# Kernel optimization log

Measured on AMD Instinct MI355X. Metric: run time of the kernel, lower is better.

The kernel has to match this reference:

```python
import jax, jax.numpy as jnp
import numpy as np

DIM = 1280
HEADS = 16
HEAD_DIM = DIM // HEADS  # 80
SEQ = 2048


def setup_inputs() -> dict:
    key = jax.random.key(0)
    ks = jax.random.split(key, 6)
    hidden_states = jax.random.normal(ks[0], (SEQ, DIM), jnp.float32)
    rotary_pos_emb = jax.random.normal(ks[1], (SEQ, HEAD_DIM // 2), jnp.float32)
    # 4 variable-length windows packed into one flat sequence
    cu_seqlens = jnp.array([0, 512, 1024, 1536, 2048], jnp.int32)
    w_scale = DIM ** -0.5
    qkv_w = jax.random.normal(ks[2], (3 * DIM, DIM), jnp.float32) * w_scale
    qkv_b = jax.random.normal(ks[3], (3 * DIM,), jnp.float32) * 0.01
    proj_w = jax.random.normal(ks[4], (DIM, DIM), jnp.float32) * w_scale
    proj_b = jax.random.normal(ks[5], (DIM,), jnp.float32) * 0.01
    return {
        "hidden_states": hidden_states,
        "rotary_pos_emb": rotary_pos_emb,
        "cu_seqlens": cu_seqlens,
        "qkv_w": qkv_w,
        "qkv_b": qkv_b,
        "proj_w": proj_w,
        "proj_b": proj_b,
    }


def _apply_rope_vision(x, freqs):
    # x: [S, H, D], freqs: [S, D//2]; matches Qwen2-VL apply_rotary_pos_emb_vision
    cos = jnp.concatenate([jnp.cos(freqs), jnp.cos(freqs)], axis=-1)[:, None, :]  # [S,1,D]
    sin = jnp.concatenate([jnp.sin(freqs), jnp.sin(freqs)], axis=-1)[:, None, :]
    x1, x2 = jnp.split(x, 2, axis=-1)
    rot = jnp.concatenate([-x2, x1], axis=-1)  # rotate_half
    return x * cos + rot * sin


def reference(hidden_states, rotary_pos_emb, cu_seqlens, qkv_w, qkv_b, proj_w, proj_b):
    S = hidden_states.shape[0]
    qkv = (hidden_states @ qkv_w.T + qkv_b).reshape(S, 3, HEADS, HEAD_DIM)
    q, k, v = qkv[:, 0], qkv[:, 1], qkv[:, 2]  # each [S, H, D]
    q = _apply_rope_vision(q, rotary_pos_emb)
    k = _apply_rope_vision(k, rotary_pos_emb)
    # varlen attention: tokens attend only within their cu_seqlens window
    seg = jnp.searchsorted(cu_seqlens[1:], jnp.arange(S), side="right")
    mask = seg[:, None] == seg[None, :]  # [S, S]
    scale = HEAD_DIM ** -0.5
    scores = jnp.einsum("shd,thd->hst", q, k) * scale  # [H, S, S]
    scores = jnp.where(mask[None, :, :], scores, jnp.finfo(scores.dtype).min)
    probs = jax.nn.softmax(scores, axis=-1)
    attn = jnp.einsum("hst,thd->shd", probs, v).reshape(S, DIM)
    return attn @ proj_w.T + proj_b
```

## Files before the change

### kernel.cpp

```cpp
#include <hip/hip_runtime.h>


typedef __attribute__((ext_vector_type(8))) short bf16x8;
typedef __attribute__((ext_vector_type(4))) float floatx4;
typedef __attribute__((ext_vector_type(4))) short short4v;
typedef __attribute__((ext_vector_type(8))) short short8v;

static __device__ __forceinline__ short f2bf(float f) {
  union { float f; unsigned u; } v; v.f = f;
  unsigned r = v.u + 0x7FFFu + ((v.u >> 16) & 1u);
  return (short)(r >> 16);
}
static __device__ __forceinline__ float bf2f(short h) {
  union { unsigned u; float f; } v;
  v.u = ((unsigned)(unsigned short)h) << 16;
  return v.f;
}

static __device__ __forceinline__ void gload16(const short* g, short* l) {
  __builtin_amdgcn_global_load_lds(
      (const __attribute__((address_space(1))) unsigned*)g,
      (__attribute__((address_space(3))) unsigned*)l, 16, 0, 0);
}

#define CVT_N1 327680
#define CVT_N2 614400
#define CVT_N3 204800
__global__ __launch_bounds__(256) void cvt3_kernel(const float* __restrict__ s1, short* __restrict__ d1,
                                                   const float* __restrict__ s2, short* __restrict__ d2,
                                                   const float* __restrict__ s3, short* __restrict__ d3) {
  int i = blockIdx.x * 256 + threadIdx.x;
  const float* s; short* d; int j;
  if (i < CVT_N1)                { s = s1; d = d1; j = i; }
  else if (i < CVT_N1 + CVT_N2)  { s = s2; d = d2; j = i - CVT_N1; }
  else                           { s = s3; d = d3; j = i - CVT_N1 - CVT_N2; }
  float4 x = ((const float4*)s)[2 * j];
  float4 y = ((const float4*)s)[2 * j + 1];
  short8v o;
  o[0] = f2bf(x.x); o[1] = f2bf(x.y); o[2] = f2bf(x.z); o[3] = f2bf(x.w);
  o[4] = f2bf(y.x); o[5] = f2bf(y.y); o[6] = f2bf(y.z); o[7] = f2bf(y.w);
  ((short8v*)d)[j] = o;
}

template <int MODE, int BM, int BN>
__global__ __launch_bounds__(256) void gemm_db(const short* __restrict__ A,
                                               const short* __restrict__ B,
                                               const float* __restrict__ bias,
                                               void* __restrict__ Cout,
                                               short* __restrict__ vt,
                                               int M, int N, int K) {
  constexpr int AR = BM / 32;
  constexpr int BR = BN / 32;
  constexpr int MI = BM / 32;
  constexpr int NJ = BN / 32;
  __shared__ short As[2][BM * 64];
  __shared__ short Bs[2][BN * 64];

  const int tid = threadIdx.x;
  const int lane = tid & 63;
  const int wave = tid >> 6;
  const int l15 = lane & 15, quad = lane >> 4;
  const int x7 = l15 & 7;

  size_t aoff[AR];
#pragma unroll
  for (int r = 0; r < AR; ++r) {
    int s = r * 256 + tid, row = s >> 3, c = (s & 7) ^ (row & 7);
    aoff[r] = (size_t)(blockIdx.y * BM + row) * K + c * 8;
  }
  size_t boff[BR];
#pragma unroll
  for (int r = 0; r < BR; ++r) {
    int s = r * 256 + tid, row = s >> 3, c = (s & 7) ^ (row & 7);
    boff[r] = (size_t)(blockIdx.x * BN + row) * K + c * 8;
  }

  const int wm = (wave >> 1) * (BM / 2);
  const int wn = (wave & 1) * (BN / 2);

  floatx4 acc[MI][NJ];
#pragma unroll
  for (int i = 0; i < MI; ++i)
#pragma unroll
    for (int j = 0; j < NJ; ++j) acc[i][j] = (floatx4){0.f, 0.f, 0.f, 0.f};

#pragma unroll
  for (int r = 0; r < AR; ++r) gload16(A + aoff[r], &As[0][(r * 256 + tid) * 8]);
#pragma unroll
  for (int r = 0; r < BR; ++r) gload16(B + boff[r], &Bs[0][(r * 256 + tid) * 8]);

  int cur = 0;
  for (int k0 = 0; k0 < K; k0 += 64) {
    __syncthreads();
    if (k0 + 64 < K) {
#pragma unroll
      for (int r = 0; r < AR; ++r)
        gload16(A + aoff[r] + k0 + 64, &As[cur ^ 1][(r * 256 + tid) * 8]);
#pragma unroll
      for (int r = 0; r < BR; ++r)
        gload16(B + boff[r] + k0 + 64, &Bs[cur ^ 1][(r * 256 + tid) * 8]);
    }
#pragma unroll
    for (int h = 0; h < 2; ++h) {
      bf16x8 af[MI], bfr[NJ];
#pragma unroll
      for (int i = 0; i < MI; ++i) {
        int row = wm + i * 16 + l15;
        af[i] = *(const bf16x8*)&As[cur][row * 64 + (((h << 2) + quad) ^ x7) * 8];
      }
#pragma unroll
      for (int j = 0; j < NJ; ++j) {
        int row = wn + j * 16 + l15;
        bfr[j] = *(const bf16x8*)&Bs[cur][row * 64 + (((h << 2) + quad) ^ x7) * 8];
      }
#pragma unroll
      for (int i = 0; i < MI; ++i)
#pragma unroll
        for (int j = 0; j < NJ; ++j)
          acc[i][j] = __builtin_amdgcn_mfma_f32_16x16x32_bf16(af[i], bfr[j], acc[i][j], 0, 0, 0);
    }
    cur ^= 1;
  }

  const int bm = blockIdx.y * BM + wm;
  const int bn = blockIdx.x * BN + wn;
#pragma unroll
  for (int j = 0; j < NJ; ++j) {
    const int col = bn + j * 16 + l15;
    const float bs = bias[col];
    if (MODE == 1) {
      float* C = (float*)Cout;
#pragma unroll
      for (int i = 0; i < MI; ++i) {
        const int row0 = bm + i * 16 + quad * 4;
#pragma unroll
        for (int e = 0; e < 4; ++e)
          C[(size_t)(row0 + e) * N + col] = acc[i][j][e] + bs;
      }
    } else {
      if (bn + j * 16 < 2560) {
        short* C = (short*)Cout;
#pragma unroll
        for (int i = 0; i < MI; ++i) {
          const int row0 = bm + i * 16 + quad * 4;
#pragma unroll
          for (int e = 0; e < 4; ++e)
            C[(size_t)(row0 + e) * 2560 + col] = f2bf(acc[i][j][e] + bs);
        }
      } else {
#pragma unroll
        for (int i = 0; i < MI; ++i) {
          const int row0 = bm + i * 16 + quad * 4;
          short4v v;
#pragma unroll
          for (int e = 0; e < 4; ++e) v[e] = f2bf(acc[i][j][e] + bs);
          *(short4v*)(vt + (size_t)(col - 2560) * 2048 + row0) = v;
        }
      }
    }
  }
}

__global__ __launch_bounds__(256) void rope_repack(const short* __restrict__ qkv,
                                                   const float* __restrict__ rot,
                                                   short* __restrict__ qp,
                                                   short* __restrict__ kp) {
  int idx = blockIdx.x * 256 + threadIdx.x;
  int d = idx % 96;
  int t = idx / 96;
  int s = t & 2047;
  int h = t >> 11;
  size_t dst = ((size_t)h * 2048 + s) * 96 + d;
  if (d < 80) {
    int base = s * 2560 + h * 80;
    int df = (d < 40) ? d : d - 40;
    int dp = (d < 40) ? d + 40 : d - 40;
    float fr = rot[s * 40 + df];
    float c = __cosf(fr), sn = __sinf(fr);
    float sgn = (d < 40) ? -1.f : 1.f;
    float xq = bf2f(qkv[base + d]);
    float pq = bf2f(qkv[base + dp]);
    float xk = bf2f(qkv[base + 1280 + d]);
    float pk = bf2f(qkv[base + 1280 + dp]);
    qp[dst] = f2bf((xq * c + sgn * pq * sn) * 0.11180339887498949f);
    kp[dst] = f2bf(xk * c + sgn * pk * sn);
  } else {
    qp[dst] = 0;
    kp[dst] = 0;
  }
}

__global__ __launch_bounds__(256) void attn_kernel(const short* __restrict__ qp,
                                                   const short* __restrict__ kp,
                                                   const short* __restrict__ vt,
                                                   short* __restrict__ attnout) {
  __shared__ short smem[29184];
  short* const Ks[2] = {smem, smem + 12288};
  short* const Vs[2] = {smem, smem + 10240};

  const int tid = threadIdx.x;
  const int lane = tid & 63;
  const int wave = tid >> 6;
  const int l15 = lane & 15, quad = lane >> 4;
  short* const Pw = smem + 20480 + wave * (16 * 136);

  const int g = blockIdx.x;
  const int hs = g & 63;
  const int grp = g >> 6;
  const int head = hs >> 2;
  const int seg = hs & 3;
  const int q0 = seg * 512 + (grp * 4 + wave) * 16;

  const short* qb = qp + ((size_t)head * 2048 + q0 + l15) * 96 + quad * 8;
  bf16x8 aq0 = *(const bf16x8*)qb;
  bf16x8 aq1 = *(const bf16x8*)(qb + 32);
  bf16x8 aq2 = *(const bf16x8*)(qb + 64);

  const short* kbase = kp + ((size_t)head * 2048 + seg * 512) * 96;
  const short* vbase = vt + (size_t)head * 80 * 2048 + seg * 512;

  floatx4 s[32];
  {
#pragma unroll
    for (int r = 0; r < 6; ++r) {
      int idx = r * 256 + tid;
      gload16(kbase + idx * 8, Ks[0] + idx * 8);
    }
#pragma unroll
    for (int c = 0; c < 4; ++c) {
      __syncthreads();
      if (c < 3) {
        const short* src = kbase + (size_t)(c + 1) * 128 * 96;
#pragma unroll
        for (int r = 0; r < 6; ++r) {
          int idx = r * 256 + tid;
          gload16(src + idx * 8, Ks[(c + 1) & 1] + idx * 8);
        }
      }
      const short* kl = Ks[c & 1];
#pragma unroll
      for (int j = 0; j < 8; ++j) {
        const short* kb = kl + (j * 16 + l15) * 96 + quad * 8;
        floatx4 acc = (floatx4){0.f, 0.f, 0.f, 0.f};
        acc = __builtin_amdgcn_mfma_f32_16x16x32_bf16(aq0, *(const bf16x8*)kb, acc, 0, 0, 0);
        acc = __builtin_amdgcn_mfma_f32_16x16x32_bf16(aq1, *(const bf16x8*)(kb + 32), acc, 0, 0, 0);
        acc = __builtin_amdgcn_mfma_f32_16x16x32_bf16(aq2, *(const bf16x8*)(kb + 64), acc, 0, 0, 0);
        s[c * 8 + j] = acc;
      }
    }
  }

  float m[4] = {-1e30f, -1e30f, -1e30f, -1e30f};
#pragma unroll
  for (int j = 0; j < 32; ++j)
#pragma unroll
    for (int e = 0; e < 4; ++e) m[e] = fmaxf(m[e], s[j][e]);
#pragma unroll
  for (int e = 0; e < 4; ++e)
#pragma unroll
    for (int o = 1; o < 16; o <<= 1) m[e] = fmaxf(m[e], __shfl_xor(m[e], o));
  float l[4] = {0.f, 0.f, 0.f, 0.f};
#pragma unroll
  for (int j = 0; j < 32; ++j)
#pragma unroll
    for (int e = 0; e < 4; ++e) {
      float p = __expf(s[j][e] - m[e]);
      s[j][e] = p;
      l[e] += p;
    }
#pragma unroll
  for (int e = 0; e < 4; ++e)
#pragma unroll
    for (int o = 1; o < 16; o <<= 1) l[e] += __shfl_xor(l[e], o);
  float inv[4];
#pragma unroll
  for (int e = 0; e < 4; ++e) inv[e] = 1.f / l[e];

  floatx4 o5[5];
#pragma unroll
  for (int t = 0; t < 5; ++t) o5[t] = (floatx4){0.f, 0.f, 0.f, 0.f};

  __syncthreads();
#pragma unroll
  for (int r = 0; r < 5; ++r) {
    int idx = r * 256 + tid;
    gload16(vbase + (size_t)(idx >> 4) * 2048 + (idx & 15) * 8, Vs[0] + idx * 8);
  }
#pragma unroll
  for (int c = 0; c < 4; ++c) {
    __syncthreads();
    if (c < 3) {
      const short* src = vbase + (c + 1) * 128;
#pragma unroll
      for (int r = 0; r < 5; ++r) {
        int idx = r * 256 + tid;
        gload16(src + (size_t)(idx >> 4) * 2048 + (idx & 15) * 8, Vs[(c + 1) & 1] + idx * 8);
      }
    }
#pragma unroll
    for (int j = 0; j < 8; ++j)
#pragma unroll
      for (int e = 0; e < 4; ++e)
        Pw[(quad * 4 + e) * 136 + j * 16 + l15] = f2bf(s[c * 8 + j][e]);
    const short* vl = Vs[c & 1];
#pragma unroll
    for (int kk = 0; kk < 4; ++kk) {
      bf16x8 ap = *(const bf16x8*)&Pw[l15 * 136 + kk * 32 + quad * 8];
#pragma unroll
      for (int t = 0; t < 5; ++t) {
        bf16x8 bv = *(const bf16x8*)&vl[(t * 16 + l15) * 128 + kk * 32 + quad * 8];
        o5[t] = __builtin_amdgcn_mfma_f32_16x16x32_bf16(ap, bv, o5[t], 0, 0, 0);
      }
    }
  }

#pragma unroll
  for (int t = 0; t < 5; ++t)
#pragma unroll
    for (int e = 0; e < 4; ++e)
      attnout[(size_t)(q0 + quad * 4 + e) * 1280 + head * 80 + t * 16 + l15] =
          f2bf(o5[t][e] * inv[e]);
}

extern "C" void kernel_launch(void* const* d_in, const int* in_sizes, int n_in,
                              void* d_out, int out_size, void* d_ws, size_t ws_size,
                              hipStream_t stream) {
  const float* hidden = (const float*)d_in[0];
  const float* rotary = (const float*)d_in[1];
  const float* qkv_w = (const float*)d_in[3];
  const float* qkv_b = (const float*)d_in[4];
  const float* proj_w = (const float*)d_in[5];
  const float* proj_b = (const float*)d_in[6];
  float* out = (float*)d_out;

  char* w = (char*)d_ws;
  short* hA   = (short*)(w + 0);
  short* w1   = (short*)(w + 5242880);
  short* w2   = (short*)(w + 15073280);
  short* qkvb = (short*)(w + 18350080);
  short* qp   = (short*)(w + 28835840);
  short* kp   = (short*)(w + 35127296);
  short* vt   = (short*)(w + 41418752);
  short* attn = (short*)(w + 46661632);

  cvt3_kernel<<<4480, 256, 0, stream>>>(hidden, hA, qkv_w, w1, proj_w, w2);

  gemm_db<2, 128, 128><<<dim3(3840 / 128, 2048 / 128), 256, 0, stream>>>(
      hA, w1, qkv_b, (void*)qkvb, vt, 2048, 3840, 1280);

  rope_repack<<<16 * 2048 * 96 / 256, 256, 0, stream>>>(qkvb, rotary, qp, kp);

  attn_kernel<<<512, 256, 0, stream>>>(qp, kp, vt, attn);

  gemm_db<1, 64, 128><<<dim3(1280 / 128, 2048 / 64), 256, 0, stream>>>(
      attn, w2, proj_b, (void*)out, nullptr, 2048, 1280, 1280);
}
```

Baseline: 171.9 us.

## Write QKV GEMM output directly into padded per-head Q/K layout, rope in place

The QKV GEMM epilogue now scatters bf16 Q and K straight into the padded [head][seq][96] buffers, and a smaller in-place rope kernel rotates the pairs there. This removes the intermediate qkv buffer and one full read/write pass. The GEMM K-tile also shrinks from 64 to 32 with a new LDS swizzle, which halves shared memory but doubles the loop iterations and barriers. The output projection moves from 64x128 to 64x64 tiles for more blocks. The epilogue stores are strided by 96 elements and less coalesced.

```diff
diff --git a/kernel.cpp b/kernel.cpp
--- a/kernel.cpp
+++ b/kernel.cpp
@@ -43,35 +43,37 @@
 }
 
 template <int MODE, int BM, int BN>
-__global__ __launch_bounds__(256) void gemm_db(const short* __restrict__ A,
-                                               const short* __restrict__ B,
-                                               const float* __restrict__ bias,
-                                               void* __restrict__ Cout,
-                                               short* __restrict__ vt,
-                                               int M, int N, int K) {
-  constexpr int AR = BM / 32;
-  constexpr int BR = BN / 32;
+__global__ __launch_bounds__(256) void gemm32(const short* __restrict__ A,
+                                              const short* __restrict__ B,
+                                              const float* __restrict__ bias,
+                                              void* __restrict__ Cout,
+                                              short* __restrict__ qp,
+                                              short* __restrict__ kp,
+                                              short* __restrict__ vt,
+                                              int M, int N, int K) {
+  constexpr int AR = BM / 64;
+  constexpr int BR = BN / 64;
   constexpr int MI = BM / 32;
   constexpr int NJ = BN / 32;
-  __shared__ short As[2][BM * 64];
-  __shared__ short Bs[2][BN * 64];
+  __shared__ short As[2][BM * 32];
+  __shared__ short Bs[2][BN * 32];
 
   const int tid = threadIdx.x;
   const int lane = tid & 63;
   const int wave = tid >> 6;
   const int l15 = lane & 15, quad = lane >> 4;
-  const int x7 = l15 & 7;
+  const int x3 = (l15 >> 1) & 3;
 
   size_t aoff[AR];
 #pragma unroll
   for (int r = 0; r < AR; ++r) {
-    int s = r * 256 + tid, row = s >> 3, c = (s & 7) ^ (row & 7);
+    int s = r * 256 + tid, row = s >> 2, c = (s & 3) ^ ((row >> 1) & 3);
     aoff[r] = (size_t)(blockIdx.y * BM + row) * K + c * 8;
   }
   size_t boff[BR];
 #pragma unroll
   for (int r = 0; r < BR; ++r) {
-    int s = r * 256 + tid, row = s >> 3, c = (s & 7) ^ (row & 7);
+    int s = r * 256 + tid, row = s >> 2, c = (s & 3) ^ ((row >> 1) & 3);
     boff[r] = (size_t)(blockIdx.x * BN + row) * K + c * 8;
   }
 
@@ -90,35 +92,32 @@
   for (int r = 0; r < BR; ++r) gload16(B + boff[r], &Bs[0][(r * 256 + tid) * 8]);
 
   int cur = 0;
-  for (int k0 = 0; k0 < K; k0 += 64) {
+  for (int k0 = 0; k0 < K; k0 += 32) {
     __syncthreads();
-    if (k0 + 64 < K) {
+    if (k0 + 32 < K) {
 #pragma unroll
       for (int r = 0; r < AR; ++r)
-        gload16(A + aoff[r] + k0 + 64, &As[cur ^ 1][(r * 256 + tid) * 8]);
+        gload16(A + aoff[r] + k0 + 32, &As[cur ^ 1][(r * 256 + tid) * 8]);
 #pragma unroll
       for (int r = 0; r < BR; ++r)
-        gload16(B + boff[r] + k0 + 64, &Bs[cur ^ 1][(r * 256 + tid) * 8]);
-    }
-#pragma unroll
-    for (int h = 0; h < 2; ++h) {
-      bf16x8 af[MI], bfr[NJ];
-#pragma unroll
-      for (int i = 0; i < MI; ++i) {
-        int row = wm + i * 16 + l15;
-        af[i] = *(const bf16x8*)&As[cur][row * 64 + (((h << 2) + quad) ^ x7) * 8];
-      }
-#pragma unroll
-      for (int j = 0; j < NJ; ++j) {
-        int row = wn + j * 16 + l15;
-        bfr[j] = *(const bf16x8*)&Bs[cur][row * 64 + (((h << 2) + quad) ^ x7) * 8];
-      }
-#pragma unroll
-      for (int i = 0; i < MI; ++i)
-#pragma unroll
-        for (int j = 0; j < NJ; ++j)
-          acc[i][j] = __builtin_amdgcn_mfma_f32_16x16x32_bf16(af[i], bfr[j], acc[i][j], 0, 0, 0);
-    }
+        gload16(B + boff[r] + k0 + 32, &Bs[cur ^ 1][(r * 256 + tid) * 8]);
+    }
+    bf16x8 af[MI], bfr[NJ];
+#pragma unroll
+    for (int i = 0; i < MI; ++i) {
+      int row = wm + i * 16 + l15;
+      af[i] = *(const bf16x8*)&As[cur][row * 32 + ((quad ^ x3) << 3)];
+    }
+#pragma unroll
+    for (int j = 0; j < NJ; ++j) {
+      int row = wn + j * 16 + l15;
+      bfr[j] = *(const bf16x8*)&Bs[cur][row * 32 + ((quad ^ x3) << 3)];
+    }
+#pragma unroll
+    for (int i = 0; i < MI; ++i)
+#pragma unroll
+      for (int j = 0; j < NJ; ++j)
+        acc[i][j] = __builtin_amdgcn_mfma_f32_16x16x32_bf16(af[i], bfr[j], acc[i][j], 0, 0, 0);
     cur ^= 1;
   }
 
@@ -139,13 +138,17 @@
       }
     } else {
       if (bn + j * 16 < 2560) {
-        short* C = (short*)Cout;
+        int head = col / 80;
+        int d = col - head * 80;
+        short* base = (head < 16)
+            ? qp + (size_t)head * 2048 * 96 + d
+            : kp + (size_t)(head - 16) * 2048 * 96 + d;
 #pragma unroll
         for (int i = 0; i < MI; ++i) {
           const int row0 = bm + i * 16 + quad * 4;
 #pragma unroll
           for (int e = 0; e < 4; ++e)
-            C[(size_t)(row0 + e) * 2560 + col] = f2bf(acc[i][j][e] + bs);
+            base[(size_t)(row0 + e) * 96] = f2bf(acc[i][j][e] + bs);
         }
       } else {
 #pragma unroll
@@ -161,32 +164,29 @@
   }
 }
 
-__global__ __launch_bounds__(256) void rope_repack(const short* __restrict__ qkv,
-                                                   const float* __restrict__ rot,
-                                                   short* __restrict__ qp,
-                                                   short* __restrict__ kp) {
+__global__ __launch_bounds__(256) void rope_ip(short* __restrict__ qp,
+                                               short* __restrict__ kp,
+                                               const float* __restrict__ rot) {
   int idx = blockIdx.x * 256 + threadIdx.x;
-  int d = idx % 96;
-  int t = idx / 96;
+  int d = idx % 48;
+  int t = idx / 48;
   int s = t & 2047;
   int h = t >> 11;
-  size_t dst = ((size_t)h * 2048 + s) * 96 + d;
-  if (d < 80) {
-    int base = s * 2560 + h * 80;
-    int df = (d < 40) ? d : d - 40;
-    int dp = (d < 40) ? d + 40 : d - 40;
-    float fr = rot[s * 40 + df];
-    float c = __cosf(fr), sn = __sinf(fr);
-    float sgn = (d < 40) ? -1.f : 1.f;
-    float xq = bf2f(qkv[base + d]);
-    float pq = bf2f(qkv[base + dp]);
-    float xk = bf2f(qkv[base + 1280 + d]);
-    float pk = bf2f(qkv[base + 1280 + dp]);
-    qp[dst] = f2bf((xq * c + sgn * pq * sn) * 0.11180339887498949f);
-    kp[dst] = f2bf(xk * c + sgn * pk * sn);
+  size_t base = ((size_t)h * 2048 + s) * 96;
+  if (d < 40) {
+    float f = rot[s * 40 + d];
+    float c = __cosf(f), sn = __sinf(f);
+    float q1 = bf2f(qp[base + d]), q2 = bf2f(qp[base + d + 40]);
+    float k1 = bf2f(kp[base + d]), k2 = bf2f(kp[base + d + 40]);
+    const float sc = 0.11180339887498949f;
+    qp[base + d]      = f2bf((q1 * c - q2 * sn) * sc);
+    qp[base + d + 40] = f2bf((q2 * c + q1 * sn) * sc);
+    kp[base + d]      = f2bf(k1 * c - k2 * sn);
+    kp[base + d + 40] = f2bf(k2 * c + k1 * sn);
   } else {
-    qp[dst] = 0;
-    kp[dst] = 0;
+    int i = d - 40;
+    *(int*)(qp + base + 80 + i * 2) = 0;
+    *(int*)(kp + base + 80 + i * 2) = 0;
   }
 }
 
@@ -337,21 +337,20 @@
   short* hA   = (short*)(w + 0);
   short* w1   = (short*)(w + 5242880);
   short* w2   = (short*)(w + 15073280);
-  short* qkvb = (short*)(w + 18350080);
-  short* qp   = (short*)(w + 28835840);
-  short* kp   = (short*)(w + 35127296);
-  short* vt   = (short*)(w + 41418752);
-  short* attn = (short*)(w + 46661632);
+  short* qp   = (short*)(w + 18350080);
+  short* kp   = (short*)(w + 24641536);
+  short* vt   = (short*)(w + 30932992);
+  short* attn = (short*)(w + 36175872);
 
   cvt3_kernel<<<4480, 256, 0, stream>>>(hidden, hA, qkv_w, w1, proj_w, w2);
 
-  gemm_db<2, 128, 128><<<dim3(3840 / 128, 2048 / 128), 256, 0, stream>>>(
-      hA, w1, qkv_b, (void*)qkvb, vt, 2048, 3840, 1280);
-
-  rope_repack<<<16 * 2048 * 96 / 256, 256, 0, stream>>>(qkvb, rotary, qp, kp);
+  gemm32<2, 128, 128><<<dim3(3840 / 128, 2048 / 128), 256, 0, stream>>>(
+      hA, w1, qkv_b, nullptr, qp, kp, vt, 2048, 3840, 1280);
+
+  rope_ip<<<16 * 2048 * 48 / 256, 256, 0, stream>>>(qp, kp, rotary);
 
   attn_kernel<<<512, 256, 0, stream>>>(qp, kp, vt, attn);
 
-  gemm_db<1, 64, 128><<<dim3(1280 / 128, 2048 / 64), 256, 0, stream>>>(
-      attn, w2, proj_b, (void*)out, nullptr, 2048, 1280, 1280);
-}
+  gemm32<1, 64, 64><<<dim3(1280 / 64, 2048 / 64), 256, 0, stream>>>(
+      attn, w2, proj_b, (void*)out, nullptr, nullptr, nullptr, 2048, 1280, 1280);
+}
```

Measured after the change: 178.2 us. +3.7%, slower.
